# Optimization experiments

Measured on AMD Instinct MI355X. Metric: run time of the kernel, lower is better.

## Reference

```python
import jax, jax.numpy as jnp
import numpy as np

B = 64
NS = [5024, 1257, 315, 80, 21]  # padded vertex counts per mesh level
K = 9                            # spiral length
LAT = 256


def _sconv(x, idx, W, b, elu=True):
    # x: [B, N, F], idx: [N, K] spiral neighbor indices -> gather, GEMM, activation, zero-pad mask
    Bq, N, _ = x.shape
    g = x[:, idx.reshape(-1), :].reshape(Bq, N, -1)  # [B, N, K*F]
    o = g @ W + b
    if elu:
        o = jax.nn.elu(o)
    return o.at[:, -1, :].set(0.0)  # zero the padding vertex


def _pool(M, x):
    # M: [M_out, M_in] dense down/up-sample matrix
    return jnp.einsum('mn,bnf->bmf', M, x)


def _forward(x, s0, s1, s2, s3, D0, D1, D2, D3, U0, U1, U2, U3,
             We0, be0, We1, be1, We2, be2, We3, be3,
             fceW, fceb, fcdW, fcdb,
             Wd0, bd0, Wd1, bd1, Wd2, bd2, Wd3, bd3):
    # encoder: spiral conv + downsample at each level
    h = _pool(D0, _sconv(x, s0, We0, be0))
    h = _pool(D1, _sconv(h, s1, We1, be1))
    h = _pool(D2, _sconv(h, s2, We2, be2))
    h = _pool(D3, _sconv(h, s3, We3, be3))
    z = h.reshape(h.shape[0], -1) @ fceW + fceb          # [B, LAT]
    # decoder: upsample + spiral conv, last conv has identity activation
    h = (z @ fcdW + fcdb).reshape(z.shape[0], NS[4], -1)  # [B, 21, 256]
    h = _sconv(_pool(U3, h), s3, Wd0, bd0)
    h = _sconv(_pool(U2, h), s2, Wd1, bd1)
    h = _sconv(_pool(U1, h), s1, Wd2, bd2)
    h = _sconv(_pool(U0, h), s0, Wd3, bd3, elu=False)
    return h  # [B, 5024, 3]


def setup_inputs() -> dict:
    key = jax.random.key(0)
    ks = iter(jax.random.split(key, 64))
    nrm = lambda shape, s=0.05: jax.random.normal(next(ks), shape, dtype=jnp.float32) * s
    d = {}
    d['x'] = jax.random.normal(next(ks), (B, NS[0], 3), dtype=jnp.float32)
    for i in range(4):
        n = NS[i]
        d[f's{i}'] = jax.random.randint(next(ks), (n, K), 0, n, dtype=jnp.int32).astype(jnp.int64)
    for i in range(4):
        d[f'D{i}'] = nrm((NS[i + 1], NS[i]))
        d[f'U{i}'] = nrm((NS[i], NS[i + 1]))
    enc = [(3, 64), (64, 64), (64, 128), (128, 256)]
    for i, (fi, fo) in enumerate(enc):
        d[f'We{i}'] = nrm((fi * K, fo))
        d[f'be{i}'] = jnp.zeros((fo,), jnp.float32)
    d['fceW'] = nrm((NS[4] * 256, LAT))
    d['fceb'] = jnp.zeros((LAT,), jnp.float32)
    d['fcdW'] = nrm((LAT, NS[4] * 256))
    d['fcdb'] = jnp.zeros((NS[4] * 256,), jnp.float32)
    dec = [(256, 128), (128, 64), (64, 64), (64, 3)]
    for i, (fi, fo) in enumerate(dec):
        d[f'Wd{i}'] = nrm((fi * K, fo))
        d[f'bd{i}'] = jnp.zeros((fo,), jnp.float32)
    return d


def reference(x, s0, s1, s2, s3, D0, D1, D2, D3, U0, U1, U2, U3,
              We0, be0, We1, be1, We2, be2, We3, be3,
              fceW, fceb, fcdW, fcdb,
              Wd0, bd0, Wd1, bd1, Wd2, bd2, Wd3, bd3):
    return _forward(x, s0, s1, s2, s3, D0, D1, D2, D3, U0, U1, U2, U3,
                    We0, be0, We1, be1, We2, be2, We3, be3,
                    fceW, fceb, fcdW, fcdb,
                    Wd0, bd0, Wd1, bd1, Wd2, bd2, Wd3, bd3)
```

## Files before the change

### kernel.cpp

```cpp
#include <hip/hip_runtime.h>
#include <math.h>

typedef __attribute__((ext_vector_type(8))) _Float16 half8;
typedef __attribute__((ext_vector_type(4))) float f32x4;
typedef unsigned long long u64;

#define BK 32

#define EPI_NAT  0
#define EPI_TR   1
#define EPI_FCD  2
#define EPI_OUT  3
#define EPI_PART 4

typedef const __attribute__((address_space(1))) void* gas1;
typedef __attribute__((address_space(3))) void* las3;

__device__ __forceinline__ void gl16(const void* g, void* l) {
    __builtin_amdgcn_global_load_lds((gas1)g, (las3)l, 16, 0, 0);
}
template<int N> __device__ __forceinline__ void vwait() {
    asm volatile("s_waitcnt vmcnt(%0)" :: "n"(N) : "memory");
}
__device__ __forceinline__ void barx() {
    asm volatile("" ::: "memory");
    __builtin_amdgcn_s_barrier();
    asm volatile("" ::: "memory");
}

template<int TBM, int OCC>
__global__ __launch_bounds__(256, OCC) void pool2_k(
    const _Float16* __restrict__ Aw, const _Float16* __restrict__ Bw,
    _Float16* __restrict__ Cp, int M, int Np, u64 c_rs)
{
    constexpr int FM  = TBM / 32;
    constexpr int LPS = TBM / 64 + 2;

    __shared__ _Float16 sA[3][TBM][BK];
    __shared__ _Float16 sB[3][128][BK];

    const int t  = threadIdx.x;
    const int m0 = blockIdx.y * TBM;
    const int f0 = blockIdx.x * 128;
    const int lane = t & 63;
    const int wid  = t >> 6;
    const int wm = wid >> 1;
    const int wf = wid & 1;
    const int lm = lane & 15;
    const int lg = lane >> 4;

    f32x4 acc[FM][4];
    #pragma unroll
    for (int i = 0; i < FM; ++i)
        #pragma unroll
        for (int j = 0; j < 4; ++j)
            acc[i][j] = (f32x4)0.0f;

    auto stage = [&](int buf, int ks) {
        #pragma unroll
        for (int j = 0; j < TBM / 64; ++j) {
            int c   = t + j * 256;
            int row = c >> 2;
            int sw  = ((c & 3) ^ ((row >> 1) & 3)) * 8;
            int rc  = m0 + row; if (rc >= M) rc = M - 1;
            gl16(Aw + (u64)rc * Np + ks * BK + sw,
                 (_Float16*)&sA[buf][0][0] + (u64)c * 8);
        }
        #pragma unroll
        for (int j = 0; j < 2; ++j) {
            int c   = t + j * 256;
            int row = c >> 2;
            int sw  = ((c & 3) ^ ((row >> 1) & 3)) * 8;
            gl16(Bw + (u64)(f0 + row) * Np + ks * BK + sw,
                 (_Float16*)&sB[buf][0][0] + (u64)c * 8);
        }
    };

    auto compute = [&](int buf) {
        const int sa = (lg ^ ((lm >> 1) & 3)) * 8;
        half8 af[FM], bf[4];
        #pragma unroll
        for (int i = 0; i < FM; ++i)
            af[i] = *(const half8*)&sA[buf][wm * (FM * 16) + i * 16 + lm][sa];
        #pragma unroll
        for (int j = 0; j < 4; ++j)
            bf[j] = *(const half8*)&sB[buf][wf * 64 + j * 16 + lm][sa];
        #pragma unroll
        for (int i = 0; i < FM; ++i)
            #pragma unroll
            for (int j = 0; j < 4; ++j)
                acc[i][j] = __builtin_amdgcn_mfma_f32_16x16x32_f16(af[i], bf[j], acc[i][j], 0, 0, 0);
    };

    const int ke = Np / BK;
    stage(0, 0);
    if (1 < ke) stage(1, 1);
    if (2 < ke) stage(2, 2);
    int cur = 0;
    for (int ks = 0; ks < ke; ++ks) {
        int rem = ke - ks;
        if (rem >= 3)      vwait<2 * LPS>();
        else if (rem == 2) vwait<LPS>();
        else               vwait<0>();
        barx();
        compute(cur);
        barx();
        if (ks + 3 < ke) stage(cur, ks + 3);
        cur = (cur == 2) ? 0 : cur + 1;
    }

    #pragma unroll
    for (int j = 0; j < 4; ++j) {
        int fl = f0 + wf * 64 + j * 16 + lm;
        #pragma unroll
        for (int i = 0; i < FM; ++i) {
            #pragma unroll
            for (int r = 0; r < 4; ++r) {
                int m = m0 + wm * (FM * 16) + i * 16 + lg * 4 + r;
                if (m < M)
                    Cp[(u64)m * c_rs + fl] = (_Float16)acc[i][j][r];
            }
        }
    }
}

template<int AMODE, int EPI, int TBM, int TBF, int WM, int WF>
__global__ __launch_bounds__(256) void gemm_k(
    const _Float16* __restrict__ Aw, u64 a_rs,
    const int* __restrict__ idx, int FiLog,
    const _Float16* __restrict__ Bw,
    const float* __restrict__ bias,
    void* __restrict__ Cp, u64 c_rs, int Mp_out,
    int M, int Np, int F, int flags, int ksp)
{
    constexpr int FM = TBM / WM / 16;
    constexpr int FF = TBF / WF / 16;
    constexpr int LPS_A = TBM / 64;
    constexpr bool BSM = (TBF < 64);
    constexpr int LPS_B = BSM ? 0 : TBF / 64;
    constexpr int LW0 = LPS_A + (BSM ? 1 : LPS_B);
    constexpr int LWX = LPS_A + LPS_B;
    constexpr int NI = (AMODE == 1) ? TBM : 2;

    __shared__ _Float16 sA[3][TBM][BK];
    __shared__ _Float16 sB[3][TBF][BK];
    __shared__ int sIdx[NI][9];

    const int t  = threadIdx.x;
    const int b  = blockIdx.z;
    const int m0 = blockIdx.y * TBM;
    const int f0 = blockIdx.x * TBF;
    const int lane = t & 63;
    const int wid  = t >> 6;
    const int wm = wid / WF;
    const int wf = wid % WF;
    const int lm = lane & 15;
    const int lg = lane >> 4;
    const int Fi = 1 << FiLog;

    f32x4 acc[FM][FF];
    #pragma unroll
    for (int i = 0; i < FM; ++i)
        #pragma unroll
        for (int j = 0; j < FF; ++j)
            acc[i][j] = (f32x4)0.0f;

    if constexpr (AMODE == 1) {
        for (int i = t; i < TBM * 9; i += 256) {
            int r = i / 9, k = i - r * 9;
            int rc = m0 + r; if (rc >= M) rc = M - 1;
            sIdx[r][k] = idx[rc * 9 + k];
        }
        __syncthreads();
    } else if constexpr (AMODE == 5) {
        if (t < 18) {
            int r = t / 9, k = t - r * 9;
            sIdx[r][k] = idx[((m0 >> 6) + r) * 9 + k];
        }
        __syncthreads();
    }

    auto stage = [&](int buf, int ks) {
        if constexpr (AMODE != 2) {
            #pragma unroll
            for (int j = 0; j < LPS_A; ++j) {
                int c   = t + j * 256;
                int row = c >> 2;
                int sw  = ((c & 3) ^ ((row >> 1) & 3)) * 8;
                int col = ks * BK + sw;
                const _Float16* src;
                if constexpr (AMODE == 3) {
                    int rc = m0 + row; if (rc >= M) rc = M - 1;
                    src = Aw + (u64)rc * Np + col;
                } else if constexpr (AMODE == 1) {
                    int k = col >> FiLog, fi = col & (Fi - 1);
                    src = Aw + (u64)sIdx[row][k] * a_rs + b * Fi + fi;
                } else if constexpr (AMODE == 4) {
                    int k = col >> FiLog, fi = col & (Fi - 1);
                    src = Aw + (u64)k * a_rs + (m0 + row) * Fi + fi;
                } else {
                    int k = col >> FiLog, fi = col & (Fi - 1);
                    int bb = (m0 + row) & 63;
                    src = Aw + (u64)sIdx[row >> 6][k] * a_rs + bb * Fi + fi;
                }
                gl16(src, &sA[buf][row][(c & 3) * 8]);
            }
        }
        if constexpr (!BSM) {
            #pragma unroll
            for (int j = 0; j < LPS_B; ++j) {
                int c   = t + j * 256;
                int row = c >> 2;
                int sw  = ((c & 3) ^ ((row >> 1) & 3)) * 8;
                gl16(Bw + (u64)(f0 + row) * Np + ks * BK + sw, &sB[buf][row][(c & 3) * 8]);
            }
        } else {
            if (wid == 0) {
                int c   = t;
                int row = c >> 2;
                int sw  = ((c & 3) ^ ((row >> 1) & 3)) * 8;
                gl16(Bw + (u64)(f0 + row) * Np + ks * BK + sw, &sB[buf][row][(c & 3) * 8]);
            }
        }
    };

    auto compute = [&](int buf) {
        const int sa = (lg ^ ((lm >> 1) & 3)) * 8;
        half8 af[FM], bf[FF];
        #pragma unroll
        for (int i = 0; i < FM; ++i)
            af[i] = *(const half8*)&sA[buf][wm * (FM * 16) + i * 16 + lm][sa];
        #pragma unroll
        for (int j = 0; j < FF; ++j)
            bf[j] = *(const half8*)&sB[buf][wf * (FF * 16) + j * 16 + lm][sa];
        #pragma unroll
        for (int i = 0; i < FM; ++i)
            #pragma unroll
            for (int j = 0; j < FF; ++j)
                acc[i][j] = __builtin_amdgcn_mfma_f32_16x16x32_f16(af[i], bf[j], acc[i][j], 0, 0, 0);
    };

    if constexpr (AMODE == 2) {
        stage(0, 0);
        {
            int row = t >> 1;
            int base = (t & 1) * 16;
            int rg = m0 + row;
            #pragma unroll
            for (int q = 0; q < 16; ++q) {
                int n = base + q;
                _Float16 val = (_Float16)0.f;
                if (rg < M && n < 27) {
                    int k = n / 3, fi = n - k * 3;
                    val = Aw[(u64)idx[rg * 9 + k] * a_rs + b * 3 + fi];
                }
                int ch = (n >> 3) ^ ((row >> 1) & 3);
                sA[0][row][ch * 8 + (n & 7)] = val;
            }
        }
        __syncthreads();
        compute(0);
    } else {
        int kb = 0, ke = Np / BK;
        if constexpr (AMODE == 4) { kb = b * ksp; ke = kb + ksp; }
        stage(0, kb);
        if (kb + 1 < ke) stage(1, kb + 1);
        if (kb + 2 < ke) stage(2, kb + 2);
        int cur = 0;
        for (int ks = kb; ks < ke; ++ks) {
            int rem = ke - ks;
            if (rem >= 3) {
                if constexpr (LW0 == LWX) vwait<2 * LW0>();
                else { if (wid == 0) vwait<2 * LW0>(); else vwait<2 * LWX>(); }
            } else if (rem == 2) {
                if constexpr (LW0 == LWX) vwait<LW0>();
                else { if (wid == 0) vwait<LW0>(); else vwait<LWX>(); }
            } else {
                vwait<0>();
            }
            barx();
            compute(cur);
            barx();
            if (ks + 3 < ke) stage(cur, ks + 3);
            cur = (cur == 2) ? 0 : cur + 1;
        }
    }

    #pragma unroll
    for (int j = 0; j < FF; ++j) {
        int fl = f0 + wf * (FF * 16) + j * 16 + lm;
        float bv = 0.f;
        if (bias != nullptr && fl < F) bv = bias[fl];
        #pragma unroll
        for (int i = 0; i < FM; ++i) {
            #pragma unroll
            for (int r = 0; r < 4; ++r) {
                int m = m0 + wm * (FM * 16) + i * 16 + lg * 4 + r;
                float v = acc[i][j][r] + bv;
                if (flags & 1) v = (v > 0.f) ? v : expm1f(v);
                if constexpr (EPI == EPI_NAT) {
                    if (m < M && fl < F)
                        ((_Float16*)Cp)[(u64)m * c_rs + fl] = (_Float16)v;
                } else if constexpr (EPI == EPI_TR) {
                    if (m < Mp_out && fl < F) {
                        float o = (m < M && !((flags & 2) && m == M - 1)) ? v : 0.f;
                        ((_Float16*)Cp)[(u64)b * c_rs + (u64)fl * Mp_out + m] = (_Float16)o;
                    }
                } else if constexpr (EPI == EPI_FCD) {
                    if (m < M && fl < F)
                        ((_Float16*)Cp)[((u64)m * 256 + (fl & 255)) * 32 + (fl >> 8)] = (_Float16)v;
                } else if constexpr (EPI == EPI_PART) {
                    if (m < M && fl < F)
                        ((float*)Cp)[(u64)b * c_rs + (u64)m * F + fl] = v;
                } else {
                    if (m < M && fl < F) {
                        int vo = m >> 6, bb = m & 63;
                        float o = ((flags & 2) && vo == Mp_out - 1) ? 0.f : v;
                        ((float*)Cp)[((u64)bb * Mp_out + vo) * 3 + fl] = o;
                    }
                }
            }
        }
    }
}

struct CvtPtrs { const float* p[18]; };

constexpr int CV_R[18]  = {1257,5024,315,1257,80,315,21,80,  64,64,128,256,256,5376,128,64,64,16};
constexpr int CV_N[18]  = {5024,1257,1257,315,315,80,80,21,  27,576,576,1152,5376,256,2304,1152,576,576};
constexpr int CV_NP[18] = {5120,1280,1280,320,320,96,96,32,  32,576,576,1152,5376,256,2304,1152,576,576};
constexpr int CV_F[18]  = {0,0,0,0,0,0,0,0,  64,64,128,256,256,5376,128,64,64,3};

constexpr u64 cv_elems(int i) { return (u64)CV_R[i] * CV_NP[i]; }
constexpr u64 cv_off(int i) { u64 o = 0; for (int j = 0; j < i; ++j) o += (cv_elems(j) + 255) & ~(u64)255; return o; }
constexpr int cv_blk(int i) { return (int)((cv_elems(i) + 255) >> 8); }
constexpr int cv_start(int i) { int s = 0; for (int j = 0; j < i; ++j) s += cv_blk(j); return s; }

__global__ __launch_bounds__(256) void cvt_all(CvtPtrs ps, _Float16* __restrict__ dst)
{
    const int bx = blockIdx.x, t = threadIdx.x;
    #pragma unroll
    for (int i = 0; i < 18; ++i) {
        if (bx >= cv_start(i) && bx < cv_start(i + 1)) {
            const u64 e = (u64)(bx - cv_start(i)) * 256 + t;
            if (e < cv_elems(i)) {
                const int NP = CV_NP[i], N = CV_N[i], Fo = CV_F[i];
                int row = (int)(e / (u64)NP);
                int col = (int)(e - (u64)row * NP);
                float v = 0.f;
                const float* s = ps.p[i];
                if (Fo == 0) { if (col < N) v = s[(u64)row * N + col]; }
                else         { if (col < N && row < Fo) v = s[(u64)col * Fo + row]; }
                dst[cv_off(i) + e] = (_Float16)v;
            }
        }
    }
}

__global__ void cvt_x(const float* __restrict__ src, _Float16* __restrict__ dst)
{
    int i = blockIdx.x * 256 + threadIdx.x;
    if (i >= 64 * 5024 * 3) return;
    int v = i / 192;
    int r = i - v * 192;
    int b = r / 3, c = r - b * 3;
    dst[i] = (_Float16)src[((u64)b * 5024 + v) * 3 + c];
}

__global__ void reduce_fce(const float* __restrict__ part, const float* __restrict__ bias,
                           _Float16* __restrict__ z)
{
    int i = blockIdx.x * 256 + threadIdx.x;
    int fl = i & 255;
    float s = bias[fl];
    #pragma unroll
    for (int p = 0; p < 8; ++p) s += part[(u64)p * 16384 + i];
    z[i] = (_Float16)s;
}

extern "C" void kernel_launch(void* const* d_in, const int* in_sizes, int n_in,
                              void* d_out, int out_size, void* d_ws, size_t ws_size,
                              hipStream_t stream)
{
    const float* x  = (const float*)d_in[0];
    const int* s0 = (const int*)d_in[1];
    const int* s1 = (const int*)d_in[2];
    const int* s2 = (const int*)d_in[3];
    const int* s3 = (const int*)d_in[4];
    const float* be0 = (const float*)d_in[14];
    const float* be1 = (const float*)d_in[16];
    const float* be2 = (const float*)d_in[18];
    const float* be3 = (const float*)d_in[20];
    const float* fceb = (const float*)d_in[22];
    const float* fcdb = (const float*)d_in[24];
    const float* bd0 = (const float*)d_in[26];
    const float* bd1 = (const float*)d_in[28];
    const float* bd2 = (const float*)d_in[30];
    const float* bd3 = (const float*)d_in[32];

    _Float16* W = (_Float16*)d_ws;
    size_t off = 0;
    auto alloc = [&](size_t e) { size_t o = off; off += (e + 255) & ~(size_t)255; return o; };

    const size_t oActV = alloc((size_t)5024 * 4096);
    const size_t oActT = alloc((size_t)4096 * 5120);
    const size_t oZ    = alloc((size_t)64 * 256);
    const size_t oPart = alloc((size_t)8 * 64 * 256 * 2);
    const size_t oU3in = alloc((size_t)16384 * 32);
    const size_t oXp   = alloc((size_t)5024 * 192);
    const size_t oCvt  = alloc((size_t)(cv_off(17) + ((cv_elems(17) + 255) & ~(u64)255)));
    auto wofs = [&](int i) { return oCvt + (size_t)cv_off(i); };

    cvt_x<<<dim3((64 * 5024 * 3 + 255) / 256), 256, 0, stream>>>(x, W + oXp);
    {
        CvtPtrs ps;
        ps.p[0] = (const float*)d_in[5];
        ps.p[1] = (const float*)d_in[6];
        ps.p[2] = (const float*)d_in[7];
        ps.p[3] = (const float*)d_in[8];
        ps.p[4] = (const float*)d_in[9];
        ps.p[5] = (const float*)d_in[10];
        ps.p[6] = (const float*)d_in[11];
        ps.p[7] = (const float*)d_in[12];
        ps.p[8] = (const float*)d_in[13];
        ps.p[9] = (const float*)d_in[15];
        ps.p[10] = (const float*)d_in[17];
        ps.p[11] = (const float*)d_in[19];
        ps.p[12] = (const float*)d_in[21];
        ps.p[13] = (const float*)d_in[23];
        ps.p[14] = (const float*)d_in[25];
        ps.p[15] = (const float*)d_in[27];
        ps.p[16] = (const float*)d_in[29];
        ps.p[17] = (const float*)d_in[31];
        cvt_all<<<dim3(cv_start(18)), 256, 0, stream>>>(ps, W + oCvt);
    }
    hipMemsetAsync(W + oU3in, 0, (size_t)16384 * 32 * sizeof(_Float16), stream);

    #define GEMM(AM, EP, BM_, BF_, WM_, WF_, gx, gy, gz, Aw_, ars_, idx_, FiL_, Bw_, bias_, Cp_, crs_, Mp_, M_, Np_, F_, fl_, ksp_) \
        gemm_k<AM, EP, BM_, BF_, WM_, WF_><<<dim3(gx, gy, gz), 256, 0, stream>>>( \
            Aw_, ars_, idx_, FiL_, Bw_, bias_, Cp_, crs_, Mp_, M_, Np_, F_, fl_, ksp_)
    #define POOL(TBM_, OCC_, gx, gy, Aw_, Bw_, Cp_, M_, Np_, crs_) \
        pool2_k<TBM_, OCC_><<<dim3(gx, gy), 256, 0, stream>>>(Aw_, Bw_, Cp_, M_, Np_, crs_)

    GEMM(2, EPI_TR, 128, 64, 2, 2, 1, 40, 64, W + oXp, 192, s0, 0,
         W + wofs(8), be0, W + oActT, (u64)64 * 5120, 5120, 5024, 32, 64, 3, 0);
    POOL(64, 3, 32, 20, W + wofs(0), W + oActT, W + oActV, 1257, 5120, 4096);
    GEMM(1, EPI_TR, 128, 64, 2, 2, 1, 10, 64, W + oActV, 4096, s1, 6,
         W + wofs(9), be1, W + oActT, (u64)64 * 1280, 1280, 1257, 576, 64, 3, 0);
    POOL(64, 3, 32, 5, W + wofs(2), W + oActT, W + oActV, 315, 1280, 4096);
    GEMM(1, EPI_TR, 128, 64, 2, 2, 2, 3, 64, W + oActV, 4096, s2, 6,
         W + wofs(10), be2, W + oActT, (u64)128 * 320, 320, 315, 576, 128, 3, 0);
    POOL(64, 3, 64, 2, W + wofs(4), W + oActT, W + oActV, 80, 320, 8192);
    GEMM(1, EPI_TR, 128, 64, 2, 2, 4, 1, 64, W + oActV, 8192, s3, 7,
         W + wofs(11), be3, W + oActT, (u64)256 * 96, 96, 80, 1152, 256, 3, 0);
    POOL(64, 3, 128, 1, W + wofs(6), W + oActT, W + oActV, 21, 96, 16384);
    GEMM(4, EPI_PART, 64, 64, 2, 2, 4, 1, 8, W + oActV, 16384, nullptr, 8,
         W + wofs(12), nullptr, W + oPart, (u64)64 * 256, 0, 64, 5376, 256, 0, 21);
    reduce_fce<<<dim3(64), 256, 0, stream>>>((const float*)(W + oPart), fceb, W + oZ);
    GEMM(3, EPI_FCD, 64, 128, 2, 2, 42, 1, 1, W + oZ, 0, nullptr, 0,
         W + wofs(13), fcdb, W + oU3in, 0, 0, 64, 256, 5376, 0, 0);
    POOL(64, 3, 128, 2, W + wofs(7), W + oU3in, W + oActV, 80, 32, 16384);
    GEMM(1, EPI_TR, 128, 64, 2, 2, 2, 1, 64, W + oActV, 16384, s3, 8,
         W + wofs(14), bd0, W + oActT, (u64)128 * 96, 96, 80, 2304, 128, 3, 0);
    POOL(64, 3, 64, 5, W + wofs(5), W + oActT, W + oActV, 315, 96, 8192);
    GEMM(1, EPI_TR, 128, 64, 2, 2, 1, 3, 64, W + oActV, 8192, s2, 7,
         W + wofs(15), bd1, W + oActT, (u64)64 * 320, 320, 315, 1152, 64, 3, 0);
    POOL(64, 3, 32, 20, W + wofs(3), W + oActT, W + oActV, 1257, 320, 4096);
    GEMM(1, EPI_TR, 128, 64, 2, 2, 1, 10, 64, W + oActV, 4096, s1, 6,
         W + wofs(16), bd2, W + oActT, (u64)64 * 1280, 1280, 1257, 576, 64, 3, 0);
    POOL(256, 2, 32, 20, W + wofs(1), W + oActT, W + oActV, 5024, 1280, 4096);
    GEMM(5, EPI_OUT, 128, 16, 4, 1, 1, 2512, 1, W + oActV, 4096, s0, 6,
         W + wofs(17), bd3, d_out, 0, 5024, 321536, 576, 3, 2, 0);
    #undef GEMM
    #undef POOL
}
```

Measured before the change: 589.6 us.

## Load pooling B operand directly into registers with triple-buffered register pipeline

The pooling GEMM kernel no longer stages the B operand (activations) through LDS. Each lane loads its MFMA B fragments from global memory into one of three register buffers, pipelined alongside the async A-tile LDS loads. The loop is unrolled by three with compile-time buffer indices so the register arrays stay static. Freeing the B shared memory lets occupancy rise to 4 for most pooling launches, and the largest upsample switches from a 256-row tile to a 128-row tile with twice the grid. The cost is more registers per thread and uncoalesced direct global reads of B, since each lane reads a 16-byte chunk from a different row.

```diff
diff --git a/kernel.cpp b/kernel.cpp
--- a/kernel.cpp
+++ b/kernel.cpp
@@ -16,6 +16,8 @@
 typedef const __attribute__((address_space(1))) void* gas1;
 typedef __attribute__((address_space(3))) void* las3;
 
+template<int I> struct ic { static constexpr int v = I; };
+
 __device__ __forceinline__ void gl16(const void* g, void* l) {
     __builtin_amdgcn_global_load_lds((gas1)g, (las3)l, 16, 0, 0);
 }
@@ -29,15 +31,14 @@
 }
 
 template<int TBM, int OCC>
-__global__ __launch_bounds__(256, OCC) void pool2_k(
+__global__ __launch_bounds__(256, OCC) void pool3_k(
     const _Float16* __restrict__ Aw, const _Float16* __restrict__ Bw,
     _Float16* __restrict__ Cp, int M, int Np, u64 c_rs)
 {
-    constexpr int FM  = TBM / 32;
-    constexpr int LPS = TBM / 64 + 2;
+    constexpr int FM = TBM / 32;
+    constexpr int LA = TBM / 64;
 
     __shared__ _Float16 sA[3][TBM][BK];
-    __shared__ _Float16 sB[3][128][BK];
 
     const int t  = threadIdx.x;
     const int m0 = blockIdx.y * TBM;
@@ -56,9 +57,13 @@
         for (int j = 0; j < 4; ++j)
             acc[i][j] = (f32x4)0.0f;
 
-    auto stage = [&](int buf, int ks) {
-        #pragma unroll
-        for (int j = 0; j < TBM / 64; ++j) {
+    half8 bB0[4], bB1[4], bB2[4];
+
+    const _Float16* Bbase = Bw + (u64)(f0 + wf * 64 + lm) * Np + lg * 8;
+
+    auto stageA = [&](int buf, int ks) {
+        #pragma unroll
+        for (int j = 0; j < LA; ++j) {
             int c   = t + j * 256;
             int row = c >> 2;
             int sw  = ((c & 3) ^ ((row >> 1) & 3)) * 8;
@@ -66,47 +71,57 @@
             gl16(Aw + (u64)rc * Np + ks * BK + sw,
                  (_Float16*)&sA[buf][0][0] + (u64)c * 8);
         }
-        #pragma unroll
-        for (int j = 0; j < 2; ++j) {
-            int c   = t + j * 256;
-            int row = c >> 2;
-            int sw  = ((c & 3) ^ ((row >> 1) & 3)) * 8;
-            gl16(Bw + (u64)(f0 + row) * Np + ks * BK + sw,
-                 (_Float16*)&sB[buf][0][0] + (u64)c * 8);
-        }
-    };
-
-    auto compute = [&](int buf) {
+    };
+    auto loadB = [&](auto bufc, int ks) {
+        constexpr int BUF = decltype(bufc)::v;
+        #pragma unroll
+        for (int j = 0; j < 4; ++j) {
+            half8 v = *(const half8*)(Bbase + (u64)j * 16 * Np + ks * BK);
+            if constexpr (BUF == 0) bB0[j] = v;
+            else if constexpr (BUF == 1) bB1[j] = v;
+            else bB2[j] = v;
+        }
+    };
+    auto computeT = [&](auto bufc) {
+        constexpr int BUF = decltype(bufc)::v;
         const int sa = (lg ^ ((lm >> 1) & 3)) * 8;
-        half8 af[FM], bf[4];
+        half8 af[FM];
         #pragma unroll
         for (int i = 0; i < FM; ++i)
-            af[i] = *(const half8*)&sA[buf][wm * (FM * 16) + i * 16 + lm][sa];
-        #pragma unroll
-        for (int j = 0; j < 4; ++j)
-            bf[j] = *(const half8*)&sB[buf][wf * 64 + j * 16 + lm][sa];
+            af[i] = *(const half8*)&sA[BUF][wm * (FM * 16) + i * 16 + lm][sa];
         #pragma unroll
         for (int i = 0; i < FM; ++i)
             #pragma unroll
-            for (int j = 0; j < 4; ++j)
-                acc[i][j] = __builtin_amdgcn_mfma_f32_16x16x32_f16(af[i], bf[j], acc[i][j], 0, 0, 0);
+            for (int j = 0; j < 4; ++j) {
+                half8 bv;
+                if constexpr (BUF == 0) bv = bB0[j];
+                else if constexpr (BUF == 1) bv = bB1[j];
+                else bv = bB2[j];
+                acc[i][j] = __builtin_amdgcn_mfma_f32_16x16x32_f16(af[i], bv, acc[i][j], 0, 0, 0);
+            }
     };
 
     const int ke = Np / BK;
-    stage(0, 0);
-    if (1 < ke) stage(1, 1);
-    if (2 < ke) stage(2, 2);
-    int cur = 0;
-    for (int ks = 0; ks < ke; ++ks) {
+    auto dostep = [&](auto bufc, int ks) {
+        constexpr int BUF = decltype(bufc)::v;
         int rem = ke - ks;
-        if (rem >= 3)      vwait<2 * LPS>();
-        else if (rem == 2) vwait<LPS>();
+        if (rem >= 3)      vwait<2 * (LA + 4)>();
+        else if (rem == 2) vwait<LA + 4>();
         else               vwait<0>();
         barx();
-        compute(cur);
+        computeT(bufc);
         barx();
-        if (ks + 3 < ke) stage(cur, ks + 3);
-        cur = (cur == 2) ? 0 : cur + 1;
+        if (ks + 3 < ke) { stageA(BUF, ks + 3); loadB(bufc, ks + 3); }
+    };
+
+    stageA(0, 0); loadB(ic<0>{}, 0);
+    if (1 < ke) { stageA(1, 1); loadB(ic<1>{}, 1); }
+    if (2 < ke) { stageA(2, 2); loadB(ic<2>{}, 2); }
+    int ks = 0;
+    while (true) {
+        dostep(ic<0>{}, ks); if (++ks >= ke) break;
+        dostep(ic<1>{}, ks); if (++ks >= ke) break;
+        dostep(ic<2>{}, ks); if (++ks >= ke) break;
     }
 
     #pragma unroll
@@ -440,35 +455,35 @@
         gemm_k<AM, EP, BM_, BF_, WM_, WF_><<<dim3(gx, gy, gz), 256, 0, stream>>>( \
             Aw_, ars_, idx_, FiL_, Bw_, bias_, Cp_, crs_, Mp_, M_, Np_, F_, fl_, ksp_)
     #define POOL(TBM_, OCC_, gx, gy, Aw_, Bw_, Cp_, M_, Np_, crs_) \
-        pool2_k<TBM_, OCC_><<<dim3(gx, gy), 256, 0, stream>>>(Aw_, Bw_, Cp_, M_, Np_, crs_)
+        pool3_k<TBM_, OCC_><<<dim3(gx, gy), 256, 0, stream>>>(Aw_, Bw_, Cp_, M_, Np_, crs_)
 
     GEMM(2, EPI_TR, 128, 64, 2, 2, 1, 40, 64, W + oXp, 192, s0, 0,
          W + wofs(8), be0, W + oActT, (u64)64 * 5120, 5120, 5024, 32, 64, 3, 0);
-    POOL(64, 3, 32, 20, W + wofs(0), W + oActT, W + oActV, 1257, 5120, 4096);
+    POOL(64, 4, 32, 20, W + wofs(0), W + oActT, W + oActV, 1257, 5120, 4096);
     GEMM(1, EPI_TR, 128, 64, 2, 2, 1, 10, 64, W + oActV, 4096, s1, 6,
          W + wofs(9), be1, W + oActT, (u64)64 * 1280, 1280, 1257, 576, 64, 3, 0);
-    POOL(64, 3, 32, 5, W + wofs(2), W + oActT, W + oActV, 315, 1280, 4096);
+    POOL(64, 4, 32, 5, W + wofs(2), W + oActT, W + oActV, 315, 1280, 4096);
     GEMM(1, EPI_TR, 128, 64, 2, 2, 2, 3, 64, W + oActV, 4096, s2, 6,
          W + wofs(10), be2, W + oActT, (u64)128 * 320, 320, 315, 576, 128, 3, 0);
-    POOL(64, 3, 64, 2, W + wofs(4), W + oActT, W + oActV, 80, 320, 8192);
+    POOL(64, 4, 64, 2, W + wofs(4), W + oActT, W + oActV, 80, 320, 8192);
     GEMM(1, EPI_TR, 128, 64, 2, 2, 4, 1, 64, W + oActV, 8192, s3, 7,
          W + wofs(11), be3, W + oActT, (u64)256 * 96, 96, 80, 1152, 256, 3, 0);
-    POOL(64, 3, 128, 1, W + wofs(6), W + oActT, W + oActV, 21, 96, 16384);
+    POOL(64, 4, 128, 1, W + wofs(6), W + oActT, W + oActV, 21, 96, 16384);
     GEMM(4, EPI_PART, 64, 64, 2, 2, 4, 1, 8, W + oActV, 16384, nullptr, 8,
          W + wofs(12), nullptr, W + oPart, (u64)64 * 256, 0, 64, 5376, 256, 0, 21);
     reduce_fce<<<dim3(64), 256, 0, stream>>>((const float*)(W + oPart), fceb, W + oZ);
     GEMM(3, EPI_FCD, 64, 128, 2, 2, 42, 1, 1, W + oZ, 0, nullptr, 0,
          W + wofs(13), fcdb, W + oU3in, 0, 0, 64, 256, 5376, 0, 0);
-    POOL(64, 3, 128, 2, W + wofs(7), W + oU3in, W + oActV, 80, 32, 16384);
+    POOL(64, 4, 128, 2, W + wofs(7), W + oU3in, W + oActV, 80, 32, 16384);
     GEMM(1, EPI_TR, 128, 64, 2, 2, 2, 1, 64, W + oActV, 16384, s3, 8,
          W + wofs(14), bd0, W + oActT, (u64)128 * 96, 96, 80, 2304, 128, 3, 0);
-    POOL(64, 3, 64, 5, W + wofs(5), W + oActT, W + oActV, 315, 96, 8192);
+    POOL(64, 4, 64, 5, W + wofs(5), W + oActT, W + oActV, 315, 96, 8192);
     GEMM(1, EPI_TR, 128, 64, 2, 2, 1, 3, 64, W + oActV, 8192, s2, 7,
          W + wofs(15), bd1, W + oActT, (u64)64 * 320, 320, 315, 1152, 64, 3, 0);
-    POOL(64, 3, 32, 20, W + wofs(3), W + oActT, W + oActV, 1257, 320, 4096);
+    POOL(64, 4, 32, 20, W + wofs(3), W + oActT, W + oActV, 1257, 320, 4096);
     GEMM(1, EPI_TR, 128, 64, 2, 2, 1, 10, 64, W + oActV, 4096, s1, 6,
          W + wofs(16), bd2, W + oActT, (u64)64 * 1280, 1280, 1257, 576, 64, 3, 0);
-    POOL(256, 2, 32, 20, W + wofs(1), W + oActT, W + oActV, 5024, 1280, 4096);
+    POOL(128, 3, 32, 40, W + wofs(1), W + oActT, W + oActV, 5024, 1280, 4096);
     GEMM(5, EPI_OUT, 128, 16, 4, 1, 1, 2512, 1, W + oActV, 4096, s0, 6,
          W + wofs(17), bd3, d_out, 0, 5024, 321536, 576, 3, 2, 0);
     #undef GEMM
```

Measured after the change: 778.6 us. 1.32x slower.
